# Optimization experiments

Measured on AMD Instinct MI355X. Metric: run time of the kernel, lower is better.

## Reference

```python
import jax, jax.numpy as jnp
import numpy as np

NUM_EXPERTS = 8
DIM = 2048
BATCH = 8192


def setup_inputs() -> dict:
    key = jax.random.key(0)
    k_x, k_ids, k_w, k_b = jax.random.split(key, 4)
    x = jax.random.normal(k_x, (BATCH, DIM), dtype=jnp.float32)
    cam_pred_ids = jax.random.randint(k_ids, (BATCH,), 0, NUM_EXPERTS, dtype=jnp.int64)
    # torch nn.Linear default init: U(-1/sqrt(in), 1/sqrt(in)); W is [out, in]
    bound = 1.0 / np.sqrt(DIM)
    W = jax.random.uniform(k_w, (NUM_EXPERTS, DIM, DIM), dtype=jnp.float32,
                           minval=-bound, maxval=bound)
    b = jax.random.uniform(k_b, (NUM_EXPERTS, DIM), dtype=jnp.float32,
                           minval=-bound, maxval=bound)
    return {"x": x, "cam_pred_ids": cam_pred_ids, "W": W, "b": b}


def reference(x, cam_pred_ids, W, b):
    # Per-sample expert routing: out[i] = x[i] + relu(x[i] @ W[e].T + b[e]),
    # where e = cam_pred_ids[i]. Vectorized as 8 full-batch GEMMs with masked
    # combine (fixed small expert count -> Python loop is structural, not data).
    h = jnp.zeros_like(x)
    for e in range(NUM_EXPERTS):
        he = jax.nn.relu(x @ W[e].T + b[e])          # [B, D]
        mask = (cam_pred_ids == e)[:, None]
        h = h + jnp.where(mask, he, jnp.zeros((), dtype=x.dtype))
    return x + h
```

## Files before the change

kernel.cpp:

```cpp
#include <hip/hip_runtime.h>
#include <hip/hip_bf16.h>
#include <stdint.h>

#define BATCH 8192
#define DIM   2048
#define NEXP  8
#define BM    128
#define BN    128
#define BK    32
#define NITER (DIM / BK)
#define MAX_TILES 72
#define NBLK  (DIM / BN)

typedef __bf16 bf16x8 __attribute__((ext_vector_type(8)));
typedef float  f32x4  __attribute__((ext_vector_type(4)));

#define XG_BYTE_OFF 40960ull
#define WB_BYTE_OFF 37789696ull
#define WS_NEED     104898560ull

#define AS1(p) ((const __attribute__((address_space(1))) void*)(p))
#define AS3(p) ((__attribute__((address_space(3))) void*)(p))

__device__ __forceinline__ unsigned f2bf2(float lo, float hi) {
    unsigned ul = __float_as_uint(lo), uh = __float_as_uint(hi);
    ul = (ul + 0x7FFFu + ((ul >> 16) & 1u)) >> 16;
    uh = (uh + 0x7FFFu + ((uh >> 16) & 1u)) >> 16;
    return (uh << 16) | ul;
}

__global__ void k_plan(const int* __restrict__ ids, int* __restrict__ ws) {
    __shared__ int sc[NEXP];
    int t = threadIdx.x;
    if (t < NEXP) sc[t] = 0;
    __syncthreads();
    for (int i = t; i < BATCH; i += 256) atomicAdd(&sc[ids[i]], 1);
    __syncthreads();
    if (t == 0) {
        int pos = 0, mt = 0;
        for (int e = 0; e < NEXP; e++) {
            int c = sc[e];
            ws[e]      = c;
            ws[16 + e] = 0;
            ws[32 + e] = pos;
            int ntl = (c + BM - 1) / BM;
            for (int tt = 0; tt < ntl; tt++) {
                ws[64  + mt] = e;
                ws[160 + mt] = pos + tt * BM;
                int v = c - tt * BM;
                ws[256 + mt] = v < BM ? v : BM;
                mt++;
            }
            pos += ntl * BM;
        }
        ws[48] = mt;
    }
}

__global__ void k_cvtW(const float4* __restrict__ W, uint2* __restrict__ Wb) {
    size_t i = (size_t)blockIdx.x * blockDim.x + threadIdx.x;
    float4 a = W[i];
    uint2 o;
    o.x = f2bf2(a.x, a.y);
    o.y = f2bf2(a.z, a.w);
    Wb[i] = o;
}

__global__ void k_gather(const float* __restrict__ x, const int* __restrict__ ids,
                         int* __restrict__ ws, unsigned short* __restrict__ xg,
                         int* __restrict__ rowmap) {
    int b = blockIdx.x;
    if (b >= BATCH) {
        int p = b - BATCH;
        int row = -1;
        for (int e = 0; e < NEXP; e++) {
            int c = ws[e];
            int pe = ((c + BM - 1) & ~(BM - 1)) - c;
            if (p < pe) { row = ws[32 + e] + c + p; break; }
            p -= pe;
        }
        if (row < 0) return;
        uint4* o = (uint4*)(xg + (size_t)row * DIM);
        uint4 z = make_uint4(0, 0, 0, 0);
        for (int t = threadIdx.x; t < DIM / 8; t += 256) o[t] = z;
        return;
    }
    __shared__ int spos;
    if (threadIdx.x == 0) {
        int e = ids[b];
        int p = ws[32 + e] + atomicAdd(&ws[16 + e], 1);
        spos = p;
        rowmap[p] = b;
    }
    __syncthreads();
    int pos = spos;
    const float4* xr = (const float4*)(x + (size_t)b * DIM);
    uint4* o = (uint4*)(xg + (size_t)pos * DIM);
    for (int t = threadIdx.x; t < DIM / 8; t += 256) {
        float4 a = xr[t * 2], b4 = xr[t * 2 + 1];
        uint4 v;
        v.x = f2bf2(a.x, a.y);  v.y = f2bf2(a.z, a.w);
        v.z = f2bf2(b4.x, b4.y); v.w = f2bf2(b4.z, b4.w);
        o[t] = v;
    }
}

__launch_bounds__(256)
__global__ void k_gemm(const unsigned short* __restrict__ xg,
                       const unsigned short* __restrict__ Wb,
                       const float* __restrict__ bias,
                       const int* __restrict__ ws, const int* __restrict__ rowmap,
                       float* __restrict__ out) {
    int mt = blockIdx.y;
    if (mt >= ws[48]) return;
    int e     = ws[64  + mt];
    int pos0  = ws[160 + mt];
    int valid = ws[256 + mt];
    int n0 = blockIdx.x * BN;

    __shared__ unsigned short lds[2][8192];

    int tid = threadIdx.x;
    int w = tid >> 6, l = tid & 63;
    int lane15 = l & 15, quad = l >> 4;
    int wave_m = (w >> 1) * 64, wave_n = (w & 1) * 64;

    const unsigned short* Abase = xg + (size_t)pos0 * DIM;
    const unsigned short* Bbase = Wb + (size_t)e * DIM * DIM + (size_t)n0 * DIM;

    int srcOff[2];
#pragma unroll
    for (int j = 0; j < 2; j++) {
        int c = w * 128 + j * 64 + l;
        int row = c >> 2, pos = c & 3;
        int q = pos ^ ((row >> 1) & 3);
        srcOff[j] = row * DIM + q * 8;
    }

    int swz = (quad ^ ((lane15 >> 1) & 3)) * 8;
    int afOff[4], bfOff[4];
#pragma unroll
    for (int mi = 0; mi < 4; mi++)
        afOff[mi] = (wave_m + mi * 16 + lane15) * BK + swz;
#pragma unroll
    for (int ni = 0; ni < 4; ni++)
        bfOff[ni] = 4096 + (wave_n + ni * 16 + lane15) * BK + swz;

    f32x4 acc[4][4];
#pragma unroll
    for (int i = 0; i < 4; i++)
#pragma unroll
        for (int j = 0; j < 4; j++) acc[i][j] = (f32x4){0.f, 0.f, 0.f, 0.f};

#define ISSUE(buf, k0)                                                          \
    do {                                                                        \
        _Pragma("unroll")                                                       \
        for (int j = 0; j < 2; j++) {                                           \
            __builtin_amdgcn_global_load_lds(                                   \
                AS1(Abase + (k0) + srcOff[j]),                                  \
                AS3(&lds[buf][w * 1024 + j * 512]), 16, 0, 0);                  \
            __builtin_amdgcn_global_load_lds(                                   \
                AS1(Bbase + (k0) + srcOff[j]),                                  \
                AS3(&lds[buf][4096 + w * 1024 + j * 512]), 16, 0, 0);           \
        }                                                                       \
    } while (0)

    ISSUE(0, 0);
    int cur = 0;
    for (int i = 0; i < NITER; ++i) {
        __syncthreads();
        if (i + 1 < NITER) {
            int k0n = (i + 1) * BK;
            ISSUE(cur ^ 1, k0n);
        }
        bf16x8 af[4], bf[4];
#pragma unroll
        for (int mi = 0; mi < 4; mi++)
            af[mi] = *(const bf16x8*)(&lds[cur][afOff[mi]]);
#pragma unroll
        for (int ni = 0; ni < 4; ni++)
            bf[ni] = *(const bf16x8*)(&lds[cur][bfOff[ni]]);
#pragma unroll
        for (int mi = 0; mi < 4; mi++)
#pragma unroll
            for (int ni = 0; ni < 4; ni++)
                acc[mi][ni] = __builtin_amdgcn_mfma_f32_16x16x32_bf16(
                    af[mi], bf[ni], acc[mi][ni], 0, 0, 0);
        cur ^= 1;
    }
#undef ISSUE

    float bv[4];
#pragma unroll
    for (int ni = 0; ni < 4; ni++)
        bv[ni] = bias[(size_t)e * DIM + n0 + wave_n + ni * 16 + lane15];
#pragma unroll
    for (int mi = 0; mi < 4; mi++) {
#pragma unroll
        for (int r = 0; r < 4; r++) {
            int rl = wave_m + mi * 16 + quad * 4 + r;
            if (rl < valid) {
                int orig = rowmap[pos0 + rl];
                const unsigned short* xrow = xg + (size_t)(pos0 + rl) * DIM + n0;
                float* orow = out + (size_t)orig * DIM + n0;
#pragma unroll
                for (int ni = 0; ni < 4; ni++) {
                    int col = wave_n + ni * 16 + lane15;
                    float xv = __uint_as_float((unsigned)xrow[col] << 16);
                    float v = acc[mi][ni][r] + bv[ni];
                    v = v > 0.f ? v : 0.f;
                    orow[col] = xv + v;
                }
            }
        }
    }
}

__global__ void k_naive(const float* __restrict__ x, const int* __restrict__ ids,
                        const float* __restrict__ W, const float* __restrict__ b,
                        float* __restrict__ out) {
    __shared__ float lx[DIM];
    int i = blockIdx.x;
    for (int t = threadIdx.x; t < DIM; t += blockDim.x) lx[t] = x[(size_t)i * DIM + t];
    __syncthreads();
    int e = ids[i];
    const float* We = W + (size_t)e * DIM * DIM;
    for (int n = threadIdx.x; n < DIM; n += blockDim.x) {
        const float* wr = We + (size_t)n * DIM;
        float acc = 0.f;
        for (int k = 0; k < DIM; k += 4) {
            float4 w4 = *(const float4*)(wr + k);
            acc += lx[k] * w4.x + lx[k + 1] * w4.y + lx[k + 2] * w4.z + lx[k + 3] * w4.w;
        }
        float v = acc + b[(size_t)e * DIM + n];
        v = v > 0.f ? v : 0.f;
        out[(size_t)i * DIM + n] = lx[n] + v;
    }
}

extern "C" void kernel_launch(void* const* d_in, const int* in_sizes, int n_in,
                              void* d_out, int out_size, void* d_ws, size_t ws_size,
                              hipStream_t stream) {
    const float* x   = (const float*)d_in[0];
    const int*   ids = (const int*)d_in[1];
    const float* W   = (const float*)d_in[2];
    const float* b   = (const float*)d_in[3];
    float* out = (float*)d_out;

    if (ws_size < WS_NEED) {
        k_naive<<<BATCH, 256, 0, stream>>>(x, ids, W, b, out);
        return;
    }

    char* wsb = (char*)d_ws;
    int*  wsi = (int*)wsb;
    unsigned short* xg = (unsigned short*)(wsb + XG_BYTE_OFF);
    unsigned short* Wb = (unsigned short*)(wsb + WB_BYTE_OFF);
    int* rowmap = wsi + 512;

    k_plan<<<1, 256, 0, stream>>>(ids, wsi);
    k_cvtW<<<(NEXP * DIM * DIM / 4) / 256, 256, 0, stream>>>((const float4*)W, (uint2*)Wb);
    k_gather<<<BATCH + 1024, 256, 0, stream>>>(x, ids, wsi, xg, rowmap);

    dim3 g(NBLK, MAX_TILES);
    k_gemm<<<g, 256, 0, stream>>>(xg, Wb, b, wsi, rowmap, out);
}
```

Baseline: 459.1 us.

## Fuse weight conversion into gather, triple-buffer GEMM loads, swizzle tile order

Merges the weight bf16 conversion kernel into the gather kernel so one launch does both, with each conversion thread handling 8 floats. The GEMM moves from a double-buffered to a triple-buffered LDS pipeline, using explicit vmcnt waits and a raw barrier so two K-steps of loads are in flight. It also remaps blocks to a 1D grid grouped by 8 M-tiles per N-block to improve L2 reuse. This costs more LDS per block, which may reduce occupancy.

```diff
diff --git a/kernel.cpp b/kernel.cpp
--- a/kernel.cpp
+++ b/kernel.cpp
@@ -11,6 +11,8 @@
 #define NITER (DIM / BK)
 #define MAX_TILES 72
 #define NBLK  (DIM / BN)
+#define NPAD  1024
+#define NCVT  16384
 
 typedef __bf16 bf16x8 __attribute__((ext_vector_type(8)));
 typedef float  f32x4  __attribute__((ext_vector_type(4)));
@@ -57,19 +59,20 @@
     }
 }
 
-__global__ void k_cvtW(const float4* __restrict__ W, uint2* __restrict__ Wb) {
-    size_t i = (size_t)blockIdx.x * blockDim.x + threadIdx.x;
-    float4 a = W[i];
-    uint2 o;
-    o.x = f2bf2(a.x, a.y);
-    o.y = f2bf2(a.z, a.w);
-    Wb[i] = o;
-}
-
-__global__ void k_gather(const float* __restrict__ x, const int* __restrict__ ids,
-                         int* __restrict__ ws, unsigned short* __restrict__ xg,
-                         int* __restrict__ rowmap) {
+__global__ void k_prep(const float* __restrict__ x, const int* __restrict__ ids,
+                       int* __restrict__ ws, unsigned short* __restrict__ xg,
+                       int* __restrict__ rowmap,
+                       const float4* __restrict__ W, uint4* __restrict__ Wb) {
     int b = blockIdx.x;
+    if (b >= BATCH + NPAD) {
+        size_t o = (size_t)(b - (BATCH + NPAD)) * 256 + threadIdx.x;
+        float4 a = W[o * 2], c = W[o * 2 + 1];
+        uint4 v;
+        v.x = f2bf2(a.x, a.y);  v.y = f2bf2(a.z, a.w);
+        v.z = f2bf2(c.x, c.y);  v.w = f2bf2(c.z, c.w);
+        Wb[o] = v;
+        return;
+    }
     if (b >= BATCH) {
         int p = b - BATCH;
         int row = -1;
@@ -96,13 +99,12 @@
     int pos = spos;
     const float4* xr = (const float4*)(x + (size_t)b * DIM);
     uint4* o = (uint4*)(xg + (size_t)pos * DIM);
-    for (int t = threadIdx.x; t < DIM / 8; t += 256) {
-        float4 a = xr[t * 2], b4 = xr[t * 2 + 1];
-        uint4 v;
-        v.x = f2bf2(a.x, a.y);  v.y = f2bf2(a.z, a.w);
-        v.z = f2bf2(b4.x, b4.y); v.w = f2bf2(b4.z, b4.w);
-        o[t] = v;
-    }
+    int t = threadIdx.x;
+    float4 a = xr[t * 2], b4 = xr[t * 2 + 1];
+    uint4 v;
+    v.x = f2bf2(a.x, a.y);   v.y = f2bf2(a.z, a.w);
+    v.z = f2bf2(b4.x, b4.y); v.w = f2bf2(b4.z, b4.w);
+    o[t] = v;
 }
 
 __launch_bounds__(256)
@@ -111,14 +113,17 @@
                        const float* __restrict__ bias,
                        const int* __restrict__ ws, const int* __restrict__ rowmap,
                        float* __restrict__ out) {
-    int mt = blockIdx.y;
+    int bid = blockIdx.x;
+    int g = bid >> 3, r = bid & 7;
+    int nb = g & 15;
+    int mt = ((g >> 4) << 3) + r;
     if (mt >= ws[48]) return;
     int e     = ws[64  + mt];
     int pos0  = ws[160 + mt];
     int valid = ws[256 + mt];
-    int n0 = blockIdx.x * BN;
-
-    __shared__ unsigned short lds[2][8192];
+    int n0 = nb * BN;
+
+    __shared__ unsigned short lds[3][8192];
 
     int tid = threadIdx.x;
     int w = tid >> 6, l = tid & 63;
@@ -166,12 +171,16 @@
     } while (0)
 
     ISSUE(0, 0);
+    ISSUE(1, BK);
     int cur = 0;
     for (int i = 0; i < NITER; ++i) {
-        __syncthreads();
-        if (i + 1 < NITER) {
-            int k0n = (i + 1) * BK;
-            ISSUE(cur ^ 1, k0n);
+        if (i + 1 < NITER) asm volatile("s_waitcnt vmcnt(4)" ::: "memory");
+        else               asm volatile("s_waitcnt vmcnt(0)" ::: "memory");
+        __builtin_amdgcn_s_barrier();
+        asm volatile("" ::: "memory");
+        if (i + 2 < NITER) {
+            int nb3 = cur + 2; if (nb3 >= 3) nb3 -= 3;
+            ISSUE(nb3, (i + 2) * BK);
         }
         bf16x8 af[4], bf[4];
 #pragma unroll
@@ -186,7 +195,7 @@
             for (int ni = 0; ni < 4; ni++)
                 acc[mi][ni] = __builtin_amdgcn_mfma_f32_16x16x32_bf16(
                     af[mi], bf[ni], acc[mi][ni], 0, 0, 0);
-        cur ^= 1;
+        if (++cur == 3) cur = 0;
     }
 #undef ISSUE
 
@@ -197,8 +206,8 @@
 #pragma unroll
     for (int mi = 0; mi < 4; mi++) {
 #pragma unroll
-        for (int r = 0; r < 4; r++) {
-            int rl = wave_m + mi * 16 + quad * 4 + r;
+        for (int r4 = 0; r4 < 4; r4++) {
+            int rl = wave_m + mi * 16 + quad * 4 + r4;
             if (rl < valid) {
                 int orig = rowmap[pos0 + rl];
                 const unsigned short* xrow = xg + (size_t)(pos0 + rl) * DIM + n0;
@@ -207,7 +216,7 @@
                 for (int ni = 0; ni < 4; ni++) {
                     int col = wave_n + ni * 16 + lane15;
                     float xv = __uint_as_float((unsigned)xrow[col] << 16);
-                    float v = acc[mi][ni][r] + bv[ni];
+                    float v = acc[mi][ni][r4] + bv[ni];
                     v = v > 0.f ? v : 0.f;
                     orow[col] = xv + v;
                 }
@@ -259,9 +268,7 @@
     int* rowmap = wsi + 512;
 
     k_plan<<<1, 256, 0, stream>>>(ids, wsi);
-    k_cvtW<<<(NEXP * DIM * DIM / 4) / 256, 256, 0, stream>>>((const float4*)W, (uint2*)Wb);
-    k_gather<<<BATCH + 1024, 256, 0, stream>>>(x, ids, wsi, xg, rowmap);
-
-    dim3 g(NBLK, MAX_TILES);
-    k_gemm<<<g, 256, 0, stream>>>(xg, Wb, b, wsi, rowmap, out);
-}
+    k_prep<<<BATCH + NPAD + NCVT, 256, 0, stream>>>(x, ids, wsi, xg, rowmap,
+                                                    (const float4*)W, (uint4*)Wb);
+    k_gemm<<<NBLK * MAX_TILES, 256, 0, stream>>>(xg, Wb, b, wsi, rowmap, out);
+}
```

Measured after the change: 468.2 us. About the same (+2.0%).
